# Performance work log

Hardware: AMD Instinct MI355X
Metric: run time of the kernel (lower is better)

Reference implementation:

```python
import jax, jax.numpy as jnp
import numpy as np

SIGMA = 4.0
KSIZE = 2 * int(4.0 * SIGMA + 0.5) + 1  # 33, anomalib AnomalyMapGenerator default


def _gauss_kernel():
    x = jnp.arange(KSIZE, dtype=jnp.float32) - (KSIZE - 1) / 2.0
    g = jnp.exp(-0.5 * (x / SIGMA) ** 2)
    return g / g.sum()


def _blur(img):
    # img: (B,1,H,W); separable Gaussian with reflect padding (kornia border_type='reflect')
    k = _gauss_kernel()
    p = (KSIZE - 1) // 2
    dn = ('NCHW', 'OIHW', 'NCHW')
    x = jnp.pad(img, ((0, 0), (0, 0), (p, p), (0, 0)), mode='reflect')
    x = jax.lax.conv_general_dilated(x, k.reshape(1, 1, KSIZE, 1), (1, 1), 'VALID', dimension_numbers=dn)
    x = jnp.pad(x, ((0, 0), (0, 0), (0, 0), (p, p)), mode='reflect')
    return jax.lax.conv_general_dilated(x, k.reshape(1, 1, 1, KSIZE), (1, 1), 'VALID', dimension_numbers=dn)


def _edist(x, y):
    # ||x-y||_2 via expanded quadratic, clamped at 0 (matches torch euclidean_dist)
    x2 = jnp.sum(x * x, axis=-1, keepdims=True)
    y2 = jnp.sum(y * y, axis=-1, keepdims=True)
    d2 = x2 - 2.0 * (x @ y.T) + y2.T
    return jnp.sqrt(jnp.clip(d2, 0.0))


def setup_inputs() -> dict:
    key = jax.random.key(0)
    k1, k2 = jax.random.split(key)
    return {
        'embedding': jax.random.normal(k1, (6272, 128), dtype=jnp.float32),
        'memory_bank': jax.random.normal(k2, (32768, 128), dtype=jnp.float32),
        'batch_size': 8,
        'width': 28,
        'height': 28,
        'out_size': 224,
        'num_neighbors': 9,
    }


def reference(embedding, memory_bank, batch_size, width, height, out_size, num_neighbors):
    N, D = embedding.shape
    M = memory_bank.shape[0]
    # --- nearest_neighbors(embedding, n_neighbors=1), euclidean metric ---
    dist = _edist(embedding, memory_bank)            # (N, M) dominant intermediate
    patch_scores = jnp.min(dist, axis=1)             # (N,)
    locations = jnp.argmin(dist, axis=1)             # (N,)
    P = N // batch_size
    patch_scores = patch_scores.reshape(batch_size, P)
    locations = locations.reshape(batch_size, P)
    # --- compute_anomaly_score (num_neighbors > 1 branch) ---
    b_idx = jnp.arange(batch_size)
    max_p = jnp.argmax(patch_scores, axis=1)                         # (B,)
    max_feat = embedding.reshape(batch_size, P, D)[b_idx, max_p]     # (B, D)
    score = patch_scores[b_idx, max_p]                               # (B,)
    nn_idx = locations[b_idx, max_p]                                 # (B,)
    nn_sample = memory_bank[nn_idx]                                  # (B, D)
    k = min(int(num_neighbors), M)
    d_nn = _edist(nn_sample, memory_bank)                            # (B, M)
    _, support = jax.lax.top_k(-d_nn, k)                             # (B, k) smallest distances
    mem_s = memory_bank[support]                                     # (B, k, D)
    qm = jnp.einsum('bd,bkd->bk', max_feat, mem_s)
    d2 = jnp.sum(max_feat * max_feat, -1, keepdims=True) - 2.0 * qm + jnp.sum(mem_s * mem_s, -1)
    dists = jnp.sqrt(jnp.clip(d2, 0.0))                              # (B, k)
    weights = (1.0 - jax.nn.softmax(dists, axis=1))[:, 0]
    pred_score = weights * score                                     # (B,)
    # --- anomaly map: bilinear upsample (align_corners=False) + Gaussian blur ---
    pm = patch_scores.reshape(batch_size, 1, width, height)
    amap = jax.image.resize(pm, (batch_size, 1, out_size, out_size), method='bilinear')
    anomaly_map = _blur(amap)
    return pred_score, anomaly_map
```

## Files before the change

### kernel.cpp

```cpp
#include <hip/hip_runtime.h>
#include <hip/hip_bf16.h>

#define N_EMB   6272
#define M_BANK  32768
#define D_DIM   128
#define KPA     256
#define KPB     128
#define BATCH   8
#define P_PATCH 784
#define GRID_WH 28
#define OUT_WH  224
#define KNN     9
#define KSIZE   33
#define KRAD    16

typedef unsigned long long ull;
typedef short bf16x8 __attribute__((ext_vector_type(8)));
typedef float f32x4  __attribute__((ext_vector_type(4)));

#define WS_MINPACK 0
#define WS_X2      50176
#define WS_Y2      75264
#define WS_PSCORE  206336
#define WS_BSCORE  231424
#define WS_BMAXP   231456
#define WS_BNN     231488
#define WS_DNN     231552
#define WS_APK     2885888
#define WS_BPK     7702784
#define WS_CAND    32868608

__device__ __forceinline__ ull umin64(ull a, ull b) { return a < b ? a : b; }
__device__ __forceinline__ ull umax64(ull a, ull b) { return a > b ? a : b; }

__device__ __forceinline__ void gload_lds16(const void* g, void* l) {
    __builtin_amdgcn_global_load_lds(
        (const __attribute__((address_space(1))) void*)g,
        (__attribute__((address_space(3))) void*)l, 16, 0, 0);
}

__global__ __launch_bounds__(256) void prep_kernel(
    const float* __restrict__ emb, const float* __restrict__ bank,
    unsigned short* __restrict__ Apk, unsigned short* __restrict__ Bpk,
    float* __restrict__ x2, float* __restrict__ y2, ull* __restrict__ minpack)
{
    const int tid = threadIdx.x;
    int gi = blockIdx.x * 256 + tid;
    if (gi < N_EMB) minpack[gi] = ~0ull;

    const int w    = blockIdx.x * 4 + (tid >> 6);
    const int lane = tid & 63;

    float2 v;
    float s;
    if (w < N_EMB) {
        const float* src = emb + (size_t)w * D_DIM;
        v = *(const float2*)&src[2 * lane];
        __hip_bfloat16 h0 = __float2bfloat16(v.x);
        __hip_bfloat16 h1 = __float2bfloat16(v.y);
        __hip_bfloat16 l0 = __float2bfloat16(v.x - __bfloat162float(h0));
        __hip_bfloat16 l1 = __float2bfloat16(v.y - __bfloat162float(h1));
        unsigned hb0 = *(unsigned short*)&h0, hb1 = *(unsigned short*)&h1;
        unsigned lb0 = *(unsigned short*)&l0, lb1 = *(unsigned short*)&l1;
        unsigned short* dst = Apk + (size_t)w * KPA;
        *(unsigned*)&dst[2 * lane]       = hb0 | (hb1 << 16);
        *(unsigned*)&dst[128 + 2 * lane] = lb0 | (lb1 << 16);
        s = fmaf(v.x, v.x, v.y * v.y);
        #pragma unroll
        for (int off = 32; off > 0; off >>= 1) s += __shfl_down(s, off, 64);
        if (lane == 0) x2[w] = s;
    } else {
        int m = w - N_EMB;
        const float* src = bank + (size_t)m * D_DIM;
        v = *(const float2*)&src[2 * lane];
        __hip_bfloat16 h0 = __float2bfloat16(v.x);
        __hip_bfloat16 h1 = __float2bfloat16(v.y);
        unsigned hb0 = *(unsigned short*)&h0, hb1 = *(unsigned short*)&h1;
        unsigned short* dst = Bpk + (size_t)m * KPB;
        *(unsigned*)&dst[2 * lane] = hb0 | (hb1 << 16);
        s = fmaf(v.x, v.x, v.y * v.y);
        #pragma unroll
        for (int off = 32; off > 0; off >>= 1) s += __shfl_down(s, off, 64);
        if (lane == 0) y2[m] = s;
    }
}

__global__ __launch_bounds__(256, 4) void mfma_min_kernel(
    const unsigned short* __restrict__ Apk, const unsigned short* __restrict__ Bpk,
    const float* __restrict__ y2, ull* __restrict__ minpack)
{
    __shared__ __align__(16) unsigned short smem[4 * 128 * 32];
    const int PAN = 128 * 32;

    const int tid  = threadIdx.x;
    const int lane = tid & 63;
    const int wave = tid >> 6;
    const int wr = wave >> 1, wc = wave & 1;
    const int n0 = blockIdx.y * 128;
    const int m0 = blockIdx.x * 128;

    const int srow = tid >> 2;
    const int sseg = tid & 3;
    const int ssw  = sseg ^ ((srow >> 1) & 3);

    const int qa = lane >> 4;
    const int ra = lane & 15;
    const int qsw = qa ^ ((ra >> 1) & 3);

    f32x4 acc[4][4];
    #pragma unroll
    for (int i = 0; i < 4; ++i)
        #pragma unroll
        for (int j = 0; j < 4; ++j)
            acc[i][j] = (f32x4){0.f, 0.f, 0.f, 0.f};

    const unsigned short* gA = Apk + (size_t)(n0 + srow) * KPA + ssw * 8;
    const unsigned short* gB = Bpk + (size_t)(m0 + srow) * KPB + ssw * 8;
    const int lof0 = srow * 32 + sseg * 8;
    const int lof1 = (srow + 64) * 32 + sseg * 8;

    #define ACOL(s) ((((s) & 1) * 128) + (((s) >> 1) * 32))

    gload_lds16(gA,            &smem[lof0]);
    gload_lds16(gA + 64 * KPA, &smem[lof1]);
    gload_lds16(gB,            &smem[2 * PAN + lof0]);
    gload_lds16(gB + 64 * KPB, &smem[2 * PAN + lof1]);

    bf16x8 bfr[4];

    #define STEP(s, VM) { \
         \
        asm volatile("s_barrier" ::: "memory"); \
        if ((s) < 7) { \
            const int ab = ((s) + 1) & 1; \
            gload_lds16(gA + ACOL((s) + 1),            &smem[ab * PAN + lof0]); \
            gload_lds16(gA + ACOL((s) + 1) + 64 * KPA, &smem[ab * PAN + lof1]); \
        } \
        if (((s) & 1) == 0 && (s) < 6) { \
            const int cn = ((s) >> 1) + 1; \
            const int bb = cn & 1; \
            gload_lds16(gB + cn * 32,            &smem[(2 + bb) * PAN + lof0]); \
            gload_lds16(gB + cn * 32 + 64 * KPB, &smem[(2 + bb) * PAN + lof1]); \
        } \
         \
        asm volatile("s_waitcnt vmcnt(" #VM ")" ::: "memory"); \
         \
        asm volatile("s_barrier" ::: "memory"); \
        const unsigned short* As = &smem[((s) & 1) * PAN]; \
        if (((s) & 1) == 0) { \
            const unsigned short* Bs = &smem[(2 + (((s) >> 1) & 1)) * PAN]; \
            _Pragma("unroll") \
            for (int j = 0; j < 4; ++j) \
                bfr[j] = *(const bf16x8*)&Bs[(wc * 64 + j * 16 + ra) * 32 + qsw * 8]; \
        } \
        { \
            bf16x8 af0 = *(const bf16x8*)&As[(wr * 64 +  0 + ra) * 32 + qsw * 8]; \
            bf16x8 af1 = *(const bf16x8*)&As[(wr * 64 + 16 + ra) * 32 + qsw * 8]; \
            _Pragma("unroll") \
            for (int j = 0; j < 4; ++j) \
                acc[0][j] = __builtin_amdgcn_mfma_f32_16x16x32_bf16(af0, bfr[j], acc[0][j], 0, 0, 0); \
            _Pragma("unroll") \
            for (int j = 0; j < 4; ++j) \
                acc[1][j] = __builtin_amdgcn_mfma_f32_16x16x32_bf16(af1, bfr[j], acc[1][j], 0, 0, 0); \
            __builtin_amdgcn_sched_barrier(0); \
            bf16x8 af2 = *(const bf16x8*)&As[(wr * 64 + 32 + ra) * 32 + qsw * 8]; \
            bf16x8 af3 = *(const bf16x8*)&As[(wr * 64 + 48 + ra) * 32 + qsw * 8]; \
            _Pragma("unroll") \
            for (int j = 0; j < 4; ++j) \
                acc[2][j] = __builtin_amdgcn_mfma_f32_16x16x32_bf16(af2, bfr[j], acc[2][j], 0, 0, 0); \
            _Pragma("unroll") \
            for (int j = 0; j < 4; ++j) \
                acc[3][j] = __builtin_amdgcn_mfma_f32_16x16x32_bf16(af3, bfr[j], acc[3][j], 0, 0, 0); \
        } \
    }

    STEP(0, 4) STEP(1, 2) STEP(2, 4) STEP(3, 2)
    STEP(4, 4) STEP(5, 2) STEP(6, 2) STEP(7, 0)
    #undef STEP
    #undef ACOL

    float y2k[4];
    unsigned mj[4];
    #pragma unroll
    for (int j = 0; j < 4; ++j) {
        const int m = m0 + wc * 64 + j * 16 + ra;
        y2k[j] = y2[m] + 1000.0f;
        mj[j]  = (unsigned)m;
    }

    ull (*red2)[32] = (ull (*)[32])smem;

    __syncthreads();

    #pragma unroll
    for (int i = 0; i < 4; ++i) {
        #pragma unroll
        for (int r = 0; r < 4; ++r) {
            const int rowl = wr * 64 + i * 16 + qa * 4 + r;
            ull mn = ~0ull;
            #pragma unroll
            for (int j = 0; j < 4; ++j) {
                float key = fmaf(-2.0f, acc[i][j][r], y2k[j]);
                ull p = ((ull)__float_as_uint(key) << 32) | mj[j];
                mn = umin64(mn, p);
            }
            red2[rowl][wc * 16 + ra] = mn;
        }
    }
    __syncthreads();
    if (tid < 128) {
        const int l = tid & 63;
        ull mn = ~0ull;
        #pragma unroll
        for (int k = 0; k < 32; ++k)
            mn = umin64(mn, red2[tid][(k + l) & 31]);
        atomicMin(&minpack[n0 + tid], mn);
    }
}

__global__ __launch_bounds__(256) void batch_argmax_kernel(
    const ull* __restrict__ minpack, const float* __restrict__ x2,
    float* __restrict__ pscore,
    float* __restrict__ bscore, int* __restrict__ bmaxp, int* __restrict__ bnn)
{
    __shared__ ull red[256];
    int b = blockIdx.x, tid = threadIdx.x;
    ull local = 0;
    for (int p = tid; p < P_PATCH; p += 256) {
        ull mp = minpack[b * P_PATCH + p];
        float key = __uint_as_float((unsigned)(mp >> 32));
        float d2 = key - 1000.0f + x2[b * P_PATCH + p];
        float sc = sqrtf(fmaxf(d2, 0.0f));
        pscore[b * P_PATCH + p] = sc;
        ull pk = ((ull)__float_as_uint(sc) << 32) | (unsigned)(p ^ 0xFFFFFFFFu);
        local = umax64(local, pk);
    }
    red[tid] = local;
    __syncthreads();
    for (int s = 128; s > 0; s >>= 1) {
        if (tid < s) red[tid] = umax64(red[tid], red[tid + s]);
        __syncthreads();
    }
    if (tid == 0) {
        ull r = red[0];
        int p = (int)(((unsigned)(r & 0xFFFFFFFFu)) ^ 0xFFFFFFFFu);
        bscore[b] = __uint_as_float((unsigned)(r >> 32));
        bmaxp[b]  = p;
        bnn[b]    = (int)(minpack[b * P_PATCH + p] & 0xFFFFFFFFu);
    }
}

__global__ __launch_bounds__(256) void dnn_kernel(
    const float* __restrict__ bank, const float* __restrict__ y2,
    const int* __restrict__ bnn, float* __restrict__ dnn)
{
    __shared__ float nn[BATCH][D_DIM];
    __shared__ float nny2[BATCH];
    int tid = threadIdx.x;
    for (int i = tid; i < BATCH * D_DIM; i += 256) {
        int b = i >> 7, d = i & 127;
        nn[b][d] = bank[(size_t)bnn[b] * D_DIM + d];
    }
    if (tid < BATCH) nny2[tid] = y2[bnn[tid]];
    __syncthreads();

    int w = tid >> 6, lane = tid & 63;
    int m = blockIdx.x * 4 + w;
    float2 v = *(const float2*)&bank[(size_t)m * D_DIM + 2 * lane];
    float part[BATCH];
    #pragma unroll
    for (int b = 0; b < BATCH; ++b)
        part[b] = fmaf(v.x, nn[b][2 * lane], v.y * nn[b][2 * lane + 1]);
    #pragma unroll
    for (int b = 0; b < BATCH; ++b) {
        float s = part[b];
        #pragma unroll
        for (int off = 32; off > 0; off >>= 1) s += __shfl_down(s, off, 64);
        if (lane == 0) {
            float d2 = nny2[b] + y2[m] - 2.0f * s;
            dnn[b * M_BANK + m] = sqrtf(fmaxf(d2, 0.0f));
        }
    }
}

__global__ __launch_bounds__(256) void topk_part_kernel(
    const float* __restrict__ dnn, ull* __restrict__ cand)
{
    __shared__ ull vals[1024];
    __shared__ ull red[256];
    const int tid = threadIdx.x;
    const int b = blockIdx.y, ch = blockIdx.x;
    const int base = ch * 1024;

    #pragma unroll
    for (int j = 0; j < 4; ++j) {
        int i = base + tid + j * 256;
        vals[tid + j * 256] = ((ull)__float_as_uint(dnn[b * M_BANK + i]) << 32) | (unsigned)i;
    }
    __syncthreads();

    for (int k = 0; k < KNN; ++k) {
        ull local = vals[tid];
        #pragma unroll
        for (int j = 1; j < 4; ++j) local = umin64(local, vals[tid + j * 256]);
        red[tid] = local;
        __syncthreads();
        for (int s = 128; s > 0; s >>= 1) {
            if (tid < s) red[tid] = umin64(red[tid], red[tid + s]);
            __syncthreads();
        }
        ull win = red[0];
        if (tid == 0) cand[(b * 32 + ch) * KNN + k] = win;
        #pragma unroll
        for (int j = 0; j < 4; ++j)
            if (vals[tid + j * 256] == win) vals[tid + j * 256] = ~0ull;
        __syncthreads();
    }
}

__global__ __launch_bounds__(256) void topk_final_kernel(
    const ull* __restrict__ cand,
    const float* __restrict__ emb, const float* __restrict__ bank,
    const float* __restrict__ x2, const float* __restrict__ y2,
    const float* __restrict__ bscore, const int* __restrict__ bmaxp,
    float* __restrict__ out)
{
    __shared__ ull vals[512];
    __shared__ ull red[256];
    __shared__ int chosen[KNN];
    __shared__ float dists[KNN];
    const int tid = threadIdx.x;
    const int b = blockIdx.x;

    vals[tid]       = (tid < 32 * KNN) ? cand[b * 32 * KNN + tid] : ~0ull;
    vals[tid + 256] = (tid + 256 < 32 * KNN) ? cand[b * 32 * KNN + tid + 256] : ~0ull;
    __syncthreads();

    for (int k = 0; k < KNN; ++k) {
        red[tid] = umin64(vals[tid], vals[tid + 256]);
        __syncthreads();
        for (int s = 128; s > 0; s >>= 1) {
            if (tid < s) red[tid] = umin64(red[tid], red[tid + s]);
            __syncthreads();
        }
        ull win = red[0];
        if (tid == 0) chosen[k] = (int)(win & 0xFFFFFFFFu);
        if (vals[tid] == win) vals[tid] = ~0ull;
        if (vals[tid + 256] == win) vals[tid + 256] = ~0ull;
        __syncthreads();
    }

    const int e = b * P_PATCH + bmaxp[b];
    if (tid < KNN) {
        const float* mf = emb + (size_t)e * D_DIM;
        const float* ms = bank + (size_t)chosen[tid] * D_DIM;
        float dot = 0.0f;
        for (int d = 0; d < D_DIM; ++d) dot = fmaf(mf[d], ms[d], dot);
        float d2 = x2[e] - 2.0f * dot + y2[chosen[tid]];
        dists[tid] = sqrtf(fmaxf(d2, 0.0f));
    }
    __syncthreads();
    if (tid == 0) {
        float mx = dists[0];
        for (int k = 1; k < KNN; ++k) mx = fmaxf(mx, dists[k]);
        float s = 0.0f;
        for (int k = 0; k < KNN; ++k) s += expf(dists[k] - mx);
        float w = 1.0f - expf(dists[0] - mx) / s;
        out[b] = w * bscore[b];
    }
}

__device__ __forceinline__ int refl224(int i) {
    if (i < 0) i = -i;
    if (i >= OUT_WH) i = 2 * (OUT_WH - 1) - i;
    return i;
}

__global__ __launch_bounds__(256) void blur_fused_kernel(
    const float* __restrict__ pscore, float* __restrict__ outp)
{
    __shared__ float g[KSIZE];
    __shared__ float ps[P_PATCH];
    __shared__ float q[GRID_WH * OUT_WH];
    __shared__ float hq[GRID_WH * OUT_WH];
    __shared__ float wrow[32][GRID_WH];

    const int tid = threadIdx.x;
    const int band = blockIdx.x;
    const int b    = blockIdx.y;

    if (tid < KSIZE) {
        float x = (tid - KRAD) * 0.25f;
        g[tid] = __expf(-0.5f * x * x);
    }
    for (int i = tid; i < P_PATCH; i += 256) ps[i] = pscore[b * P_PATCH + i];
    __syncthreads();
    if (tid == 0) {
        float s = 0.0f;
        for (int i = 0; i < KSIZE; ++i) s += g[i];
        float inv = 1.0f / s;
        for (int i = 0; i < KSIZE; ++i) g[i] *= inv;
    }
    __syncthreads();

    for (int i = tid; i < GRID_WH * OUT_WH; i += 256) {
        int gy = i / OUT_WH, x = i - gy * OUT_WH;
        float cx = (2 * x - 7) * 0.0625f;
        int ix = (int)floorf(cx); float fx = cx - ix;
        int x0 = min(max(ix, 0), GRID_WH - 1), x1 = min(max(ix + 1, 0), GRID_WH - 1);
        q[i] = ps[gy * GRID_WH + x0] * (1.0f - fx) + ps[gy * GRID_WH + x1] * fx;
    }

    if (tid < 32) {
        int y = band * 32 + tid;
        for (int gy = 0; gy < GRID_WH; ++gy) wrow[tid][gy] = 0.0f;
        for (int t = 0; t < KSIZE; ++t) {
            int yy = refl224(y - KRAD + t);
            float cy = (2 * yy - 7) * 0.0625f;
            int iy = (int)floorf(cy); float fy = cy - iy;
            int y0 = min(max(iy, 0), GRID_WH - 1), y1 = min(max(iy + 1, 0), GRID_WH - 1);
            wrow[tid][y0] += g[t] * (1.0f - fy);
            wrow[tid][y1] += g[t] * fy;
        }
    }
    __syncthreads();

    for (int i = tid; i < GRID_WH * OUT_WH; i += 256) {
        int gy = i / OUT_WH, x = i - gy * OUT_WH;
        float s = 0.0f;
        #pragma unroll
        for (int t = 0; t < KSIZE; ++t)
            s = fmaf(g[t], q[gy * OUT_WH + refl224(x - KRAD + t)], s);
        hq[i] = s;
    }
    __syncthreads();

    const int yl = tid >> 3;
    const int xbase = (tid & 7) * 28;
    const int y = band * 32 + yl;
    float* orow = outp + ((size_t)b * OUT_WH + y) * OUT_WH;
    for (int i = 0; i < 28; ++i) {
        int x = xbase + i;
        float s = 0.0f;
        #pragma unroll
        for (int gy = 0; gy < GRID_WH; ++gy)
            s = fmaf(wrow[yl][gy], hq[gy * OUT_WH + x], s);
        orow[x] = s;
    }
}

extern "C" void kernel_launch(void* const* d_in, const int* in_sizes, int n_in,
                              void* d_out, int out_size, void* d_ws, size_t ws_size,
                              hipStream_t stream) {
    const float* emb  = (const float*)d_in[0];
    const float* bank = (const float*)d_in[1];
    float* out = (float*)d_out;

    char* ws = (char*)d_ws;
    ull*   minpack = (ull*)(ws + WS_MINPACK);
    float* x2      = (float*)(ws + WS_X2);
    float* y2      = (float*)(ws + WS_Y2);
    float* pscore  = (float*)(ws + WS_PSCORE);
    float* bscore  = (float*)(ws + WS_BSCORE);
    int*   bmaxp   = (int*)(ws + WS_BMAXP);
    int*   bnn     = (int*)(ws + WS_BNN);
    float* dnn     = (float*)(ws + WS_DNN);
    unsigned short* Apk = (unsigned short*)(ws + WS_APK);
    unsigned short* Bpk = (unsigned short*)(ws + WS_BPK);
    ull*   cand    = (ull*)(ws + WS_CAND);

    prep_kernel<<<(N_EMB + M_BANK) / 4, 256, 0, stream>>>(emb, bank, Apk, Bpk, x2, y2, minpack);
    {
        dim3 grid(M_BANK / 128, N_EMB / 128);
        mfma_min_kernel<<<grid, 256, 0, stream>>>(Apk, Bpk, y2, minpack);
    }
    batch_argmax_kernel<<<BATCH, 256, 0, stream>>>(minpack, x2, pscore, bscore, bmaxp, bnn);
    dnn_kernel<<<M_BANK / 4, 256, 0, stream>>>(bank, y2, bnn, dnn);
    {
        dim3 grid(32, BATCH);
        topk_part_kernel<<<grid, 256, 0, stream>>>(dnn, cand);
    }
    topk_final_kernel<<<BATCH, 256, 0, stream>>>(cand, emb, bank, x2, y2, bscore, bmaxp, out);
    {
        dim3 grid(OUT_WH / 32, BATCH);
        blur_fused_kernel<<<grid, 256, 0, stream>>>(pscore, out + BATCH);
    }
}
```

Before: 267.3 us.

## Fuse argmax into blur kernel and distance computation into top-k partial kernel

```diff
diff --git a/kernel.cpp b/kernel.cpp
--- a/kernel.cpp
+++ b/kernel.cpp
@@ -21,11 +21,9 @@
 #define WS_MINPACK 0
 #define WS_X2      50176
 #define WS_Y2      75264
-#define WS_PSCORE  206336
 #define WS_BSCORE  231424
 #define WS_BMAXP   231456
 #define WS_BNN     231488
-#define WS_DNN     231552
 #define WS_APK     2885888
 #define WS_BPK     7702784
 #define WS_CAND    32868608
@@ -218,84 +216,141 @@
     }
 }
 
-__global__ __launch_bounds__(256) void batch_argmax_kernel(
+__device__ __forceinline__ int refl224(int i) {
+    if (i < 0) i = -i;
+    if (i >= OUT_WH) i = 2 * (OUT_WH - 1) - i;
+    return i;
+}
+
+__global__ __launch_bounds__(256) void blur_argmax_kernel(
     const ull* __restrict__ minpack, const float* __restrict__ x2,
-    float* __restrict__ pscore,
-    float* __restrict__ bscore, int* __restrict__ bmaxp, int* __restrict__ bnn)
+    float* __restrict__ bscore, int* __restrict__ bmaxp, int* __restrict__ bnn,
+    float* __restrict__ outp)
 {
+    __shared__ float g[KSIZE];
+    __shared__ float ps[P_PATCH];
+    __shared__ float q[GRID_WH * OUT_WH];
+    __shared__ float hq[GRID_WH * OUT_WH];
+    __shared__ float wrow[32][GRID_WH];
     __shared__ ull red[256];
-    int b = blockIdx.x, tid = threadIdx.x;
+
+    const int tid = threadIdx.x;
+    const int band = blockIdx.x;
+    const int b    = blockIdx.y;
+
+    if (tid < KSIZE) {
+        float x = (tid - KRAD) * 0.25f;
+        g[tid] = __expf(-0.5f * x * x);
+    }
     ull local = 0;
-    for (int p = tid; p < P_PATCH; p += 256) {
-        ull mp = minpack[b * P_PATCH + p];
+    for (int i = tid; i < P_PATCH; i += 256) {
+        ull mp = minpack[b * P_PATCH + i];
         float key = __uint_as_float((unsigned)(mp >> 32));
-        float d2 = key - 1000.0f + x2[b * P_PATCH + p];
+        float d2 = key - 1000.0f + x2[b * P_PATCH + i];
         float sc = sqrtf(fmaxf(d2, 0.0f));
-        pscore[b * P_PATCH + p] = sc;
-        ull pk = ((ull)__float_as_uint(sc) << 32) | (unsigned)(p ^ 0xFFFFFFFFu);
+        ps[i] = sc;
+        ull pk = ((ull)__float_as_uint(sc) << 32) | (unsigned)(i ^ 0xFFFFFFFFu);
         local = umax64(local, pk);
     }
     red[tid] = local;
     __syncthreads();
+    if (tid == 0) {
+        float s = 0.0f;
+        for (int i = 0; i < KSIZE; ++i) s += g[i];
+        float inv = 1.0f / s;
+        for (int i = 0; i < KSIZE; ++i) g[i] *= inv;
+    }
     for (int s = 128; s > 0; s >>= 1) {
         if (tid < s) red[tid] = umax64(red[tid], red[tid + s]);
         __syncthreads();
     }
-    if (tid == 0) {
+    if (band == 0 && tid == 0) {
         ull r = red[0];
         int p = (int)(((unsigned)(r & 0xFFFFFFFFu)) ^ 0xFFFFFFFFu);
         bscore[b] = __uint_as_float((unsigned)(r >> 32));
         bmaxp[b]  = p;
         bnn[b]    = (int)(minpack[b * P_PATCH + p] & 0xFFFFFFFFu);
     }
-}
-
-__global__ __launch_bounds__(256) void dnn_kernel(
+
+    for (int i = tid; i < GRID_WH * OUT_WH; i += 256) {
+        int gy = i / OUT_WH, x = i - gy * OUT_WH;
+        float cx = (2 * x - 7) * 0.0625f;
+        int ix = (int)floorf(cx); float fx = cx - ix;
+        int x0 = min(max(ix, 0), GRID_WH - 1), x1 = min(max(ix + 1, 0), GRID_WH - 1);
+        q[i] = ps[gy * GRID_WH + x0] * (1.0f - fx) + ps[gy * GRID_WH + x1] * fx;
+    }
+
+    if (tid < 32) {
+        int y = band * 32 + tid;
+        for (int gy = 0; gy < GRID_WH; ++gy) wrow[tid][gy] = 0.0f;
+        for (int t = 0; t < KSIZE; ++t) {
+            int yy = refl224(y - KRAD + t);
+            float cy = (2 * yy - 7) * 0.0625f;
+            int iy = (int)floorf(cy); float fy = cy - iy;
+            int y0 = min(max(iy, 0), GRID_WH - 1), y1 = min(max(iy + 1, 0), GRID_WH - 1);
+            wrow[tid][y0] += g[t] * (1.0f - fy);
+            wrow[tid][y1] += g[t] * fy;
+        }
+    }
+    __syncthreads();
+
+    for (int i = tid; i < GRID_WH * OUT_WH; i += 256) {
+        int gy = i / OUT_WH, x = i - gy * OUT_WH;
+        float s = 0.0f;
+        #pragma unroll
+        for (int t = 0; t < KSIZE; ++t)
+            s = fmaf(g[t], q[gy * OUT_WH + refl224(x - KRAD + t)], s);
+        hq[i] = s;
+    }
+    __syncthreads();
+
+    const int yl = tid >> 3;
+    const int xbase = (tid & 7) * 28;
+    const int y = band * 32 + yl;
+    float* orow = outp + ((size_t)b * OUT_WH + y) * OUT_WH;
+    for (int i = 0; i < 28; ++i) {
+        int x = xbase + i;
+        float s = 0.0f;
+        #pragma unroll
+        for (int gy = 0; gy < GRID_WH; ++gy)
+            s = fmaf(wrow[yl][gy], hq[gy * OUT_WH + x], s);
+        orow[x] = s;
+    }
+}
+
+__global__ __launch_bounds__(256) void dnn_topk_kernel(
     const float* __restrict__ bank, const float* __restrict__ y2,
-    const int* __restrict__ bnn, float* __restrict__ dnn)
+    const int* __restrict__ bnn, ull* __restrict__ cand)
 {
-    __shared__ float nn[BATCH][D_DIM];
-    __shared__ float nny2[BATCH];
-    int tid = threadIdx.x;
-    for (int i = tid; i < BATCH * D_DIM; i += 256) {
-        int b = i >> 7, d = i & 127;
-        nn[b][d] = bank[(size_t)bnn[b] * D_DIM + d];
-    }
-    if (tid < BATCH) nny2[tid] = y2[bnn[tid]];
-    __syncthreads();
-
-    int w = tid >> 6, lane = tid & 63;
-    int m = blockIdx.x * 4 + w;
-    float2 v = *(const float2*)&bank[(size_t)m * D_DIM + 2 * lane];
-    float part[BATCH];
-    #pragma unroll
-    for (int b = 0; b < BATCH; ++b)
-        part[b] = fmaf(v.x, nn[b][2 * lane], v.y * nn[b][2 * lane + 1]);
-    #pragma unroll
-    for (int b = 0; b < BATCH; ++b) {
-        float s = part[b];
-        #pragma unroll
-        for (int off = 32; off > 0; off >>= 1) s += __shfl_down(s, off, 64);
-        if (lane == 0) {
-            float d2 = nny2[b] + y2[m] - 2.0f * s;
-            dnn[b * M_BANK + m] = sqrtf(fmaxf(d2, 0.0f));
-        }
-    }
-}
-
-__global__ __launch_bounds__(256) void topk_part_kernel(
-    const float* __restrict__ dnn, ull* __restrict__ cand)
-{
+    __shared__ float nn[D_DIM];
+    __shared__ float nny2s;
     __shared__ ull vals[1024];
     __shared__ ull red[256];
     const int tid = threadIdx.x;
     const int b = blockIdx.y, ch = blockIdx.x;
     const int base = ch * 1024;
 
-    #pragma unroll
-    for (int j = 0; j < 4; ++j) {
-        int i = base + tid + j * 256;
-        vals[tid + j * 256] = ((ull)__float_as_uint(dnn[b * M_BANK + i]) << 32) | (unsigned)i;
+    const int nni = bnn[b];
+    if (tid < D_DIM) nn[tid] = bank[(size_t)nni * D_DIM + tid];
+    if (tid == D_DIM) nny2s = y2[nni];
+    __syncthreads();
+
+    const int w = tid >> 6, lane = tid & 63;
+    const float nn0 = nn[2 * lane], nn1 = nn[2 * lane + 1];
+    const float ny2 = nny2s;
+    #pragma unroll 2
+    for (int k = 0; k < 256; ++k) {
+        const int row = w * 256 + k;
+        const int m = base + row;
+        float2 v = *(const float2*)&bank[(size_t)m * D_DIM + 2 * lane];
+        float s = fmaf(v.x, nn0, v.y * nn1);
+        #pragma unroll
+        for (int off = 32; off > 0; off >>= 1) s += __shfl_down(s, off, 64);
+        if (lane == 0) {
+            float d2 = ny2 + y2[m] - 2.0f * s;
+            float sc = sqrtf(fmaxf(d2, 0.0f));
+            vals[row] = ((ull)__float_as_uint(sc) << 32) | (unsigned)m;
+        }
     }
     __syncthreads();
 
@@ -370,85 +425,6 @@
     }
 }
 
-__device__ __forceinline__ int refl224(int i) {
-    if (i < 0) i = -i;
-    if (i >= OUT_WH) i = 2 * (OUT_WH - 1) - i;
-    return i;
-}
-
-__global__ __launch_bounds__(256) void blur_fused_kernel(
-    const float* __restrict__ pscore, float* __restrict__ outp)
-{
-    __shared__ float g[KSIZE];
-    __shared__ float ps[P_PATCH];
-    __shared__ float q[GRID_WH * OUT_WH];
-    __shared__ float hq[GRID_WH * OUT_WH];
-    __shared__ float wrow[32][GRID_WH];
-
-    const int tid = threadIdx.x;
-    const int band = blockIdx.x;
-    const int b    = blockIdx.y;
-
-    if (tid < KSIZE) {
-        float x = (tid - KRAD) * 0.25f;
-        g[tid] = __expf(-0.5f * x * x);
-    }
-    for (int i = tid; i < P_PATCH; i += 256) ps[i] = pscore[b * P_PATCH + i];
-    __syncthreads();
-    if (tid == 0) {
-        float s = 0.0f;
-        for (int i = 0; i < KSIZE; ++i) s += g[i];
-        float inv = 1.0f / s;
-        for (int i = 0; i < KSIZE; ++i) g[i] *= inv;
-    }
-    __syncthreads();
-
-    for (int i = tid; i < GRID_WH * OUT_WH; i += 256) {
-        int gy = i / OUT_WH, x = i - gy * OUT_WH;
-        float cx = (2 * x - 7) * 0.0625f;
-        int ix = (int)floorf(cx); float fx = cx - ix;
-        int x0 = min(max(ix, 0), GRID_WH - 1), x1 = min(max(ix + 1, 0), GRID_WH - 1);
-        q[i] = ps[gy * GRID_WH + x0] * (1.0f - fx) + ps[gy * GRID_WH + x1] * fx;
-    }
-
-    if (tid < 32) {
-        int y = band * 32 + tid;
-        for (int gy = 0; gy < GRID_WH; ++gy) wrow[tid][gy] = 0.0f;
-        for (int t = 0; t < KSIZE; ++t) {
-            int yy = refl224(y - KRAD + t);
-            float cy = (2 * yy - 7) * 0.0625f;
-            int iy = (int)floorf(cy); float fy = cy - iy;
-            int y0 = min(max(iy, 0), GRID_WH - 1), y1 = min(max(iy + 1, 0), GRID_WH - 1);
-            wrow[tid][y0] += g[t] * (1.0f - fy);
-            wrow[tid][y1] += g[t] * fy;
-        }
-    }
-    __syncthreads();
-
-    for (int i = tid; i < GRID_WH * OUT_WH; i += 256) {
-        int gy = i / OUT_WH, x = i - gy * OUT_WH;
-        float s = 0.0f;
-        #pragma unroll
-        for (int t = 0; t < KSIZE; ++t)
-            s = fmaf(g[t], q[gy * OUT_WH + refl224(x - KRAD + t)], s);
-        hq[i] = s;
-    }
-    __syncthreads();
-
-    const int yl = tid >> 3;
-    const int xbase = (tid & 7) * 28;
-    const int y = band * 32 + yl;
-    float* orow = outp + ((size_t)b * OUT_WH + y) * OUT_WH;
-    for (int i = 0; i < 28; ++i) {
-        int x = xbase + i;
-        float s = 0.0f;
-        #pragma unroll
-        for (int gy = 0; gy < GRID_WH; ++gy)
-            s = fmaf(wrow[yl][gy], hq[gy * OUT_WH + x], s);
-        orow[x] = s;
-    }
-}
-
 extern "C" void kernel_launch(void* const* d_in, const int* in_sizes, int n_in,
                               void* d_out, int out_size, void* d_ws, size_t ws_size,
                               hipStream_t stream) {
@@ -460,11 +436,9 @@
     ull*   minpack = (ull*)(ws + WS_MINPACK);
     float* x2      = (float*)(ws + WS_X2);
     float* y2      = (float*)(ws + WS_Y2);
-    float* pscore  = (float*)(ws + WS_PSCORE);
     float* bscore  = (float*)(ws + WS_BSCORE);
     int*   bmaxp   = (int*)(ws + WS_BMAXP);
     int*   bnn     = (int*)(ws + WS_BNN);
-    float* dnn     = (float*)(ws + WS_DNN);
     unsigned short* Apk = (unsigned short*)(ws + WS_APK);
     unsigned short* Bpk = (unsigned short*)(ws + WS_BPK);
     ull*   cand    = (ull*)(ws + WS_CAND);
@@ -474,15 +448,13 @@
         dim3 grid(M_BANK / 128, N_EMB / 128);
         mfma_min_kernel<<<grid, 256, 0, stream>>>(Apk, Bpk, y2, minpack);
     }
-    batch_argmax_kernel<<<BATCH, 256, 0, stream>>>(minpack, x2, pscore, bscore, bmaxp, bnn);
-    dnn_kernel<<<M_BANK / 4, 256, 0, stream>>>(bank, y2, bnn, dnn);
+    {
+        dim3 grid(OUT_WH / 32, BATCH);
+        blur_argmax_kernel<<<grid, 256, 0, stream>>>(minpack, x2, bscore, bmaxp, bnn, out + BATCH);
+    }
     {
         dim3 grid(32, BATCH);
-        topk_part_kernel<<<grid, 256, 0, stream>>>(dnn, cand);
+        dnn_topk_kernel<<<grid, 256, 0, stream>>>(bank, y2, bnn, cand);
     }
     topk_final_kernel<<<BATCH, 256, 0, stream>>>(cand, emb, bank, x2, y2, bscore, bmaxp, out);
-    {
-        dim3 grid(OUT_WH / 32, BATCH);
-        blur_fused_kernel<<<grid, 256, 0, stream>>>(pscore, out + BATCH);
-    }
-}
+}
```

Result: slower. 399.4 us (+49.4%).
